# Performance work log

Hardware: AMD Instinct MI355X
Metric: run time of the kernel (lower is better)

Reference implementation:

```python
import jax, jax.numpy as jnp
import numpy as np

EPS = 1e-8
NUM_CELLS = 20
MEM_SIZE = 300
MLP_SIZE = 300
DECAY = 0.98
T, B, H = 512, 128, MEM_SIZE


def setup_inputs() -> dict:
    key = jax.random.key(0)
    ks = jax.random.split(key, 8)
    s = 0.05
    return {
        "hidden_states": jax.random.normal(ks[0], (T, B, H), jnp.float32),
        "input_mask": jnp.ones((T, B), jnp.float32),
        # entity_mlp: H -> MLP_SIZE -> 1
        "We1": jax.random.normal(ks[1], (H, MLP_SIZE), jnp.float32) * s,
        "be1": jnp.zeros((MLP_SIZE,), jnp.float32),
        "We2": jax.random.normal(ks[2], (MLP_SIZE, 1), jnp.float32) * s,
        "be2": jnp.zeros((1,), jnp.float32),
        # sim_mlp: 3H+1 -> MLP_SIZE -> 1
        "Ws1": jax.random.normal(ks[3], (3 * H + 1, MLP_SIZE), jnp.float32) * s,
        "bs1": jnp.zeros((MLP_SIZE,), jnp.float32),
        "Ws2": jax.random.normal(ks[4], (MLP_SIZE, 1), jnp.float32) * s,
        "bs2": jnp.zeros((1,), jnp.float32),
        # U_key: 2H -> H
        "Wu": jax.random.normal(ks[5], (2 * H, H), jnp.float32) * s,
        "bu": jnp.zeros((H,), jnp.float32),
    }


def _forward(hidden_states, input_mask, We1, be1, We2, be2, Ws1, bs1, Ws2, bs2, Wu, bu):
    Tn, Bn, Hn = hidden_states.shape
    M = NUM_CELLS
    # eval-mode random tie-break noise for pick_overwrite_cell (uniform(0.01, 1))
    noise = jax.random.uniform(jax.random.key(42), (Tn, Bn, M), jnp.float32, 0.01, 1.0)

    mem0 = jnp.zeros((Bn, M, Hn), hidden_states.dtype)
    usage0 = jnp.zeros((Bn, M), hidden_states.dtype)

    def step(carry, xs):
        mem, usage = carry
        h, mask, nz = xs  # h: [B,H], mask: [B], nz: [B,M]
        # entity probability: softmax([0, s]) == sigmoid(s)
        ent_score = jnp.maximum(h @ We1 + be1, 0.0) @ We2 + be2  # [B,1]
        ent_prob = jax.nn.sigmoid(ent_score) * mask[:, None]     # [B,1]
        qb = jnp.broadcast_to(h[:, None, :], (Bn, M, Hn))        # [B,M,H]
        pair = jnp.concatenate([mem, qb, qb * mem, usage[..., None]], axis=-1)  # [B,M,3H+1]
        sim = (jnp.maximum(pair @ Ws1 + bs1, 0.0) @ Ws2 + bs2)[..., 0]          # [B,M]
        # coref / overwrite distribution over cells + base slot
        comb = jnp.concatenate([sim, jnp.zeros((Bn, 1), sim.dtype)], axis=1)    # [B,M+1]
        coref_mask = (usage > 0).astype(sim.dtype)
        mult = jnp.concatenate([coref_mask, jnp.ones((Bn, 1), sim.dtype)], axis=1)
        comb = comb * mult + (1.0 - mult) * (-10000.0)
        probs = jax.nn.softmax(comb, axis=1)
        masked = probs * mult
        norm = masked / (jnp.sum(masked, axis=1, keepdims=True) + EPS)
        co = ent_prob * norm
        indv = co[:, :M]                 # [B,M] coref probs
        ow_base = co[:, M:M + 1]         # [B,1] overwrite prob mass
        # pick overwrite cell (eval branch: hard argmax with random tie-break)
        nsim = jax.nn.softmax(sim, axis=-1)
        ow_score = (usage == 0.0).astype(sim.dtype) * nsim * 100000.0 + (1.0 - usage)
        maxv = jnp.max(ow_score, axis=-1, keepdims=True)
        idx = jnp.argmax(nz * (ow_score == maxv).astype(sim.dtype), axis=-1)
        onehot = jax.nn.one_hot(idx, M, dtype=sim.dtype)
        ow = ow_base * onehot            # [B,M]
        # memory candidate + blended update
        cand = jnp.tanh(jnp.concatenate([qb, mem], axis=-1) @ Wu + bu)  # [B,M,H]
        new_mem = (ow[..., None] * qb
                   + (1.0 - ow - indv)[..., None] * mem
                   + indv[..., None] * cand)
        new_usage = jnp.minimum(1.0, ow + indv + DECAY * usage)
        outs = (ent_prob * (1.0 - EPS) + EPS,
                new_usage,
                indv * (1.0 - EPS) + EPS,
                ow * (1.0 - EPS) + EPS)
        return (new_mem, new_usage), outs

    (_, _), (ent, usage_seq, coref, overwrite) = jax.lax.scan(
        step, (mem0, usage0), (hidden_states, input_mask, noise))
    return ent, usage_seq, coref, overwrite


def reference(hidden_states, input_mask, We1, be1, We2, be2, Ws1, bs1, Ws2, bs2, Wu, bu):
    # returns (ent [T,B,1], usage [T,B,M], coref [T,B,M], overwrite [T,B,M])
    return _forward(hidden_states, input_mask, We1, be1, We2, be2,
                    Ws1, bs1, Ws2, bs2, Wu, bu)
```

## Files before the change

kernel.cpp:

```cpp
#include <hip/hip_runtime.h>
#include <math.h>

#define T_STEPS 512
#define BATCH   128
#define HDIM    300
#define M       20
#define M2      10

#define WS_SYNC_FLOATS 16384
#define HB1_OFF  WS_SYNC_FLOATS
#define NTB      (T_STEPS * BATCH)
#define HBUF_FLOATS ((size_t)NTB * HDIM)
#define HWU_OFF  (HB1_OFF + HBUF_FLOATS)
#define ENT_OFF  (HWU_OFF + HBUF_FLOATS)
#define WS_NEED_BYTES ((size_t)(ENT_OFF + NTB) * 4)

__device__ __forceinline__ unsigned rotl32(unsigned v, int r) {
    return (v << r) | (v >> (32 - r));
}

__device__ float jax_noise(unsigned i) {
#pragma clang fp contract(off)
    unsigned x0 = 0u;
    unsigned x1 = i;
    const unsigned ks0 = 0u, ks1 = 42u, ks2 = 0u ^ 42u ^ 0x1BD11BDAu;
    x0 += ks0; x1 += ks1;
    x0 += x1; x1 = rotl32(x1, 13); x1 ^= x0;
    x0 += x1; x1 = rotl32(x1, 15); x1 ^= x0;
    x0 += x1; x1 = rotl32(x1, 26); x1 ^= x0;
    x0 += x1; x1 = rotl32(x1, 6);  x1 ^= x0;
    x0 += ks1; x1 += ks2 + 1u;
    x0 += x1; x1 = rotl32(x1, 17); x1 ^= x0;
    x0 += x1; x1 = rotl32(x1, 29); x1 ^= x0;
    x0 += x1; x1 = rotl32(x1, 16); x1 ^= x0;
    x0 += x1; x1 = rotl32(x1, 24); x1 ^= x0;
    x0 += ks2; x1 += ks0 + 2u;
    x0 += x1; x1 = rotl32(x1, 13); x1 ^= x0;
    x0 += x1; x1 = rotl32(x1, 15); x1 ^= x0;
    x0 += x1; x1 = rotl32(x1, 26); x1 ^= x0;
    x0 += x1; x1 = rotl32(x1, 6);  x1 ^= x0;
    x0 += ks0; x1 += ks1 + 3u;
    x0 += x1; x1 = rotl32(x1, 17); x1 ^= x0;
    x0 += x1; x1 = rotl32(x1, 29); x1 ^= x0;
    x0 += x1; x1 = rotl32(x1, 16); x1 ^= x0;
    x0 += x1; x1 = rotl32(x1, 24); x1 ^= x0;
    x0 += ks1; x1 += ks2 + 4u;
    x0 += x1; x1 = rotl32(x1, 13); x1 ^= x0;
    x0 += x1; x1 = rotl32(x1, 15); x1 ^= x0;
    x0 += x1; x1 = rotl32(x1, 26); x1 ^= x0;
    x0 += x1; x1 = rotl32(x1, 6);  x1 ^= x0;
    x0 += ks2; x1 += ks0 + 5u;

    const unsigned bits = x0 ^ x1;
    const unsigned fb = (bits >> 9) | 0x3f800000u;
    float f = __uint_as_float(fb) - 1.0f;
    const float span = 1.0f - 0.01f;
    float v = f * span;
    v = v + 0.01f;
    return fmaxf(0.01f, v);
}

#define FOR5(X) X(0) X(1) X(2) X(3) X(4)
#define FOR8(X) X(0) X(1) X(2) X(3) X(4) X(5) X(6) X(7)

__global__ void __launch_bounds__(320)
pre_kernel(const float* __restrict__ hs,  const float* __restrict__ msk,
           const float* __restrict__ We1, const float* __restrict__ be1,
           const float* __restrict__ We2, const float* __restrict__ be2,
           const float* __restrict__ Ws1, const float* __restrict__ bs1,
           const float* __restrict__ Wu,  const float* __restrict__ bu,
           float* __restrict__ out, float* __restrict__ ws)
{
    __shared__ __align__(16) float sh_h[8][HDIM];
    __shared__ float sh_ent[5][8];

    float* hb1buf = ws + HB1_OFF;
    float* hwubuf = ws + HWU_OFF;
    float* entbuf = ws + ENT_OFF;

    const int tb0  = blockIdx.x * 8;
    const int tid  = threadIdx.x;
    const int wave = tid >> 6;
    const int lane = tid & 63;
    const int c    = tid;
    const bool act = c < HDIM;

    for (int i = tid; i < 8 * HDIM; i += 320)
        sh_h[i / HDIM][i % HDIM] = hs[(size_t)tb0 * HDIM + i];
    __syncthreads();

    float be1c = 0.f, we2c = 0.f, bs1c = 0.f, buc = 0.f;
    if (act) { be1c = be1[c]; we2c = We2[c]; bs1c = bs1[c]; buc = bu[c]; }

#define DECL(r) float a1_##r = 0.f, ae_##r = 0.f, au_##r = 0.f;
    FOR8(DECL)
#undef DECL
    if (act) {
        const float* q1 = Ws1 + 90000 + c;
        const float* qe = We1 + c;
        const float* qu = Wu + c;
        for (int k = 0; k < HDIM; k += 4) {
            const float* r1 = q1 + k * 300;
            const float* re = qe + k * 300;
            const float* ru = qu + k * 300;
            float w10 = r1[0], w11 = r1[300], w12 = r1[600], w13 = r1[900];
            float e0  = re[0], e1  = re[300], e2  = re[600], e3  = re[900];
            float u0  = ru[0], u1  = ru[300], u2  = ru[600], u3  = ru[900];
#define ACC(r) { float4 h4 = *(const float4*)&sh_h[r][k]; \
            a1_##r += h4.x * w10 + h4.y * w11 + h4.z * w12 + h4.w * w13; \
            ae_##r += h4.x * e0  + h4.y * e1  + h4.z * e2  + h4.w * e3;  \
            au_##r += h4.x * u0  + h4.y * u1  + h4.z * u2  + h4.w * u3; }
            FOR8(ACC)
#undef ACC
        }
#define WR(r) { hb1buf[(size_t)(tb0 + r) * HDIM + c] = a1_##r + bs1c; \
                hwubuf[(size_t)(tb0 + r) * HDIM + c] = au_##r + buc; }
        FOR8(WR)
#undef WR
    }
#define ENT(r) { float er = act ? (fmaxf(ae_##r + be1c, 0.f) * we2c) : 0.f; \
    for (int off = 32; off; off >>= 1) er += __shfl_xor(er, off, 64); \
    if (lane == 0) sh_ent[wave][r] = er; }
    FOR8(ENT)
#undef ENT
    __syncthreads();
    if (tid < 8) {
        float es = sh_ent[0][tid] + sh_ent[1][tid] + sh_ent[2][tid]
                 + sh_ent[3][tid] + sh_ent[4][tid] + be2[0];
        float entp = (1.0f / (1.0f + expf(-es))) * msk[tb0 + tid];
        entbuf[tb0 + tid] = entp;
        out[tb0 + tid] = entp * (1.0f - 1e-8f) + 1e-8f;
    }
}

__global__ void __launch_bounds__(640, 3)
wm_fast(const float* __restrict__ hs,
        const float* __restrict__ We2,
        const float* __restrict__ Ws1,
        const float* __restrict__ Ws2,
        const float* __restrict__ bs2,
        const float* __restrict__ Wu,
        float* __restrict__ out,
        float* __restrict__ ws)
{
    __shared__ __align__(16) float sh_mem[M2][HDIM];
    __shared__ __align__(16) float sh_h[HDIM];
    __shared__ __align__(16) float sh_usage[17408];
    __shared__ float sh_simpart[10][5];
    __shared__ float sh_ow[M];
    __shared__ float sh_indv[M];

    const float* hb1buf = ws + HB1_OFF;
    const float* hwubuf = ws + HWU_OFF;
    const float* entbuf = ws + ENT_OFF;

    const int bid   = blockIdx.x;
    const int b     = bid & 127;
    const int jhalf = bid >> 7;
    const int jb2   = jhalf * 10;
    const int pbase = 10 - jb2;
    const int pbid  = bid ^ 128;

    float*    vals_me = ws + (size_t)bid * 16;
    float*    vals_p  = ws + (size_t)pbid * 16;
    unsigned* flag_me = (unsigned*)(ws + 4096) + (size_t)bid * 16;
    unsigned* flag_p  = (unsigned*)(ws + 4096) + (size_t)pbid * 16;

    const int tid  = threadIdx.x;
    const int wave = tid >> 6;
    const int lane = tid & 63;

    const bool lower   = tid < 320;
    const int  c       = lower ? tid : (tid - 320);
    const bool act     = c < HDIM;
    const int  rowbase = lower ? 0 : 5;

    for (int idx = tid; idx < M2 * HDIM; idx += 640) ((float*)sh_mem)[idx] = 0.0f;
    if (tid < M) sh_usage[tid] = 0.0f;

    const float bs2v = bs2[0];
    float ws2c = 0.f, w900c = 0.f;
    if (act) { ws2c = Ws2[c]; w900c = Ws1[900 * 300 + c]; }
    __syncthreads();

    for (int t = 0; t < T_STEPS; ++t) {
        const int tb = t * BATCH + b;

        if (!lower && act) sh_h[c] = hs[(size_t)tb * HDIM + c];
        __syncthreads();

        const float hb1v = act ? hb1buf[(size_t)tb * HDIM + c] : 0.f;
        const float hwuv = act ? hwubuf[(size_t)tb * HDIM + c] : 0.f;
        const float hreg = act ? sh_h[c] : 0.f;

#define DECL_ACC(jj) float aS_##jj = 0.f, aC_##jj = 0.f;
        FOR5(DECL_ACC)
#undef DECL_ACC
        if (act) {
            const float* qa = Ws1 + c;
            const float* qc = Ws1 + 180000 + c;
            const float* qu = Wu + 90000 + c;
            float A0 = qa[0], A1v = qa[300], A2 = qa[600], A3 = qa[900];
            float C0 = qc[0], C1 = qc[300], C2 = qc[600], C3 = qc[900];
            float U0 = qu[0], U1 = qu[300], U2 = qu[600], U3 = qu[900];
            for (int k = 0; k < HDIM; k += 4) {
                const int kn = (k + 4 < HDIM) ? (k + 4) : 0;
                const float* na = qa + kn * 300;
                const float* nc = qc + kn * 300;
                const float* nu = qu + kn * 300;
                float NA0 = na[0], NA1 = na[300], NA2 = na[600], NA3 = na[900];
                float NC0 = nc[0], NC1 = nc[300], NC2 = nc[600], NC3 = nc[900];
                float NU0 = nu[0], NU1 = nu[300], NU2 = nu[600], NU3 = nu[900];

                float4 h4 = *(const float4*)&sh_h[k];
                float w0 = fmaf(h4.x, C0, A0);
                float w1 = fmaf(h4.y, C1, A1v);
                float w2 = fmaf(h4.z, C2, A2);
                float w3 = fmaf(h4.w, C3, A3);
#define ACC_J(jj) { \
                float4 mv = *(const float4*)&sh_mem[rowbase + jj][k]; \
                aS_##jj += mv.x * w0 + mv.y * w1 + mv.z * w2 + mv.w * w3; \
                aC_##jj += mv.x * U0 + mv.y * U1 + mv.z * U2 + mv.w * U3; }
                FOR5(ACC_J)
#undef ACC_J
                A0 = NA0; A1v = NA1; A2 = NA2; A3 = NA3;
                C0 = NC0; C1 = NC1; C2 = NC2; C3 = NC3;
                U0 = NU0; U1 = NU1; U2 = NU2; U3 = NU3;
            }
        }

        {
            const int gbase = jb2 + rowbase;
#define SIMF(jj) { \
            float v = act ? (fmaxf(aS_##jj + hb1v + sh_usage[gbase + jj] * w900c, 0.0f) * ws2c) : 0.0f; \
            for (int off = 32; off; off >>= 1) v += __shfl_xor(v, off, 64); \
            if (lane == 0) sh_simpart[wave][jj] = v; }
            FOR5(SIMF)
#undef SIMF
        }
        __syncthreads();

        if (wave == 0) {
            float sown = 0.f;
            if (lane < M2) {
                const int wb = (lane < 5) ? 0 : 5;
                const int rr = (lane < 5) ? lane : (lane - 5);
                sown = sh_simpart[wb][rr] + sh_simpart[wb + 1][rr] + sh_simpart[wb + 2][rr]
                     + sh_simpart[wb + 3][rr] + sh_simpart[wb + 4][rr];
                __hip_atomic_store(&vals_me[lane], sown, __ATOMIC_RELAXED,
                                   __HIP_MEMORY_SCOPE_AGENT);
            }
            if (lane == 0) {
                __hip_atomic_store(flag_me, (unsigned)(t + 1), __ATOMIC_RELEASE,
                                   __HIP_MEMORY_SCOPE_AGENT);
                while (__hip_atomic_load(flag_p, __ATOMIC_ACQUIRE,
                                         __HIP_MEMORY_SCOPE_AGENT) < (unsigned)(t + 1))
                    __builtin_amdgcn_s_sleep(1);
            }
            float pvv = 0.f;
            if (lane >= pbase && lane < pbase + M2)
                pvv = __hip_atomic_load(&vals_p[lane - pbase], __ATOMIC_ACQUIRE,
                                        __HIP_MEMORY_SCOPE_AGENT);
            const float myv = __shfl(sown, lane - jb2, 64);

            const bool actc = lane < M;
            const bool own  = actc && (lane >= jb2) && (lane < jb2 + M2);
            float simj = -INFINITY, usg = 0.0f;
            if (actc) {
                simj = (own ? myv : pvv) + bs2v;
                usg  = sh_usage[lane];
            }
            const float entp = entbuf[tb];

            const float coref = (actc && usg > 0.0f) ? 1.0f : 0.0f;
            float comb = actc ? ((usg > 0.0f) ? simj : -10000.0f) : -INFINITY;
            float mx = comb;
            for (int off = 32; off; off >>= 1) mx = fmaxf(mx, __shfl_xor(mx, off, 64));
            mx = fmaxf(mx, 0.0f);
            float e = actc ? expf(comb - mx) : 0.0f;
            const float eM = expf(0.0f - mx);
            float den = e;
            for (int off = 32; off; off >>= 1) den += __shfl_xor(den, off, 64);
            den += eM;
            const float prob  = e / den;
            const float probM = eM / den;
            float masked = prob * coref;
            float msum = masked;
            for (int off = 32; off; off >>= 1) msum += __shfl_xor(msum, off, 64);
            msum += probM;
            const float dn = msum + 1e-8f;
            const float normj = masked / dn;
            const float normM = probM / dn;
            const float indv = actc ? (entp * normj) : 0.0f;
            const float ow_base = entp * normM;

            float nmx = simj;
            for (int off = 32; off; off >>= 1) nmx = fmaxf(nmx, __shfl_xor(nmx, off, 64));
            float ne = actc ? expf(simj - nmx) : 0.0f;
            float ns = ne;
            for (int off = 32; off; off >>= 1) ns += __shfl_xor(ns, off, 64);
            const float nsim = ne / ns;

            float ows = actc ? (((usg == 0.0f) ? nsim * 100000.0f : 0.0f) + (1.0f - usg))
                             : -INFINITY;
            float mv = ows;
            for (int off = 32; off; off >>= 1) mv = fmaxf(mv, __shfl_xor(mv, off, 64));

            float key = 0.0f;
            if (actc && ows == mv) key = jax_noise((unsigned)(tb * M + lane));
            float bv = actc ? key : -1.0f;
            int bi = actc ? lane : 1023;
            for (int off = 32; off; off >>= 1) {
                float ov = __shfl_xor(bv, off, 64);
                int oi = __shfl_xor(bi, off, 64);
                if (ov > bv || (ov == bv && oi < bi)) { bv = ov; bi = oi; }
            }
            const float ow = (actc && lane == bi) ? ow_base : 0.0f;
            const float nu = fminf(1.0f, (ow + indv) + 0.98f * usg);

            if (actc) {
                sh_ow[lane] = ow;
                sh_indv[lane] = indv;
                sh_usage[lane] = nu;
            }
            if (own) {
                const int base = tb * M + lane;
                out[65536 + base]   = nu;
                out[1376256 + base] = indv * (1.0f - 1e-8f) + 1e-8f;
                out[2686976 + base] = ow * (1.0f - 1e-8f) + 1e-8f;
            }
        }
        __syncthreads();

        if (act) {
            const int gbase = jb2 + rowbase;
#define DUPD(jj) { \
            const float owj = sh_ow[gbase + jj]; \
            const float inj = sh_indv[gbase + jj]; \
            const float cd  = tanhf(aC_##jj + hwuv); \
            const float mo  = sh_mem[rowbase + jj][c]; \
            sh_mem[rowbase + jj][c] = owj * hreg + (1.0f - owj - inj) * mo + inj * cd; }
            FOR5(DUPD)
#undef DUPD
        }
    }
}

__global__ void __launch_bounds__(640, 3)
wm_kernel(const float* __restrict__ hs, const float* __restrict__ msk,
          const float* __restrict__ We1, const float* __restrict__ be1,
          const float* __restrict__ We2, const float* __restrict__ be2,
          const float* __restrict__ Ws1, const float* __restrict__ bs1,
          const float* __restrict__ Ws2, const float* __restrict__ bs2,
          const float* __restrict__ Wu,  const float* __restrict__ bu,
          float* __restrict__ out, float* __restrict__ ws)
{
    __shared__ __align__(16) float sh_mem[M2][HDIM];
    __shared__ __align__(16) float sh_h[HDIM];
    __shared__ __align__(16) float sh_hb1[HDIM];
    __shared__ __align__(16) float sh_hwu[HDIM];
    __shared__ __align__(16) float sh_usage[16384];
    __shared__ float sh_simpart[10][5];
    __shared__ float sh_entpart[5];
    __shared__ float sh_ow[M];
    __shared__ float sh_indv[M];

    const int bid   = blockIdx.x;
    const int b     = bid & 127;
    const int jhalf = bid >> 7;
    const int jb2   = jhalf * 10;
    const int pbase = 10 - jb2;
    const int pbid  = bid ^ 128;

    float*    vals_me = ws + (size_t)bid * 16;
    float*    vals_p  = ws + (size_t)pbid * 16;
    unsigned* flag_me = (unsigned*)(ws + 4096) + (size_t)bid * 16;
    unsigned* flag_p  = (unsigned*)(ws + 4096) + (size_t)pbid * 16;

    const int tid  = threadIdx.x;
    const int wave = tid >> 6;
    const int lane = tid & 63;

    const bool lower   = tid < 320;
    const int  c       = lower ? tid : (tid - 320);
    const bool act     = c < HDIM;
    const int  rowbase = lower ? 0 : 5;

    for (int idx = tid; idx < M2 * HDIM; idx += 640) ((float*)sh_mem)[idx] = 0.0f;
    if (tid < M) sh_usage[tid] = 0.0f;

    const float be2v = be2[0];
    const float bs2v = bs2[0];
    float bs1c = 0.f, be1c = 0.f, we2c = 0.f, ws2c = 0.f, w900c = 0.f, buc = 0.f;
    if (act) {
        ws2c  = Ws2[c];
        w900c = Ws1[900 * 300 + c];
        if (lower) { bs1c = bs1[c]; be1c = be1[c]; we2c = We2[c]; }
        else       { buc = bu[c]; }
    }
    __syncthreads();

    for (int t = 0; t < T_STEPS; ++t) {
        const int tb = t * BATCH + b;

        if (!lower && act) sh_h[c] = hs[(size_t)tb * HDIM + c];
        __syncthreads();

        float hb1reg = 0.f, hwureg = 0.f;
        if (lower) {
            float a1 = 0.f, ae = 0.f;
            if (act) {
                const float* q  = Ws1 + 90000 + c;
                const float* qe = We1 + c;
                float Q0 = q[0], Q1 = q[300], Q2 = q[600], Q3 = q[900];
                float E0 = qe[0], E1 = qe[300], E2 = qe[600], E3 = qe[900];
                for (int k = 0; k < HDIM; k += 4) {
                    const int kn = (k + 4 < HDIM) ? (k + 4) : 0;
                    const float* nq = q + kn * 300;
                    const float* nE = qe + kn * 300;
                    float NQ0 = nq[0], NQ1 = nq[300], NQ2 = nq[600], NQ3 = nq[900];
                    float NE0 = nE[0], NE1 = nE[300], NE2 = nE[600], NE3 = nE[900];
                    float4 h4 = *(const float4*)&sh_h[k];
                    a1 += h4.x * Q0 + h4.y * Q1 + h4.z * Q2 + h4.w * Q3;
                    ae += h4.x * E0 + h4.y * E1 + h4.z * E2 + h4.w * E3;
                    Q0 = NQ0; Q1 = NQ1; Q2 = NQ2; Q3 = NQ3;
                    E0 = NE0; E1 = NE1; E2 = NE2; E3 = NE3;
                }
            }
            float er = act ? (fmaxf(ae + be1c, 0.0f) * we2c) : 0.0f;
            for (int off = 32; off; off >>= 1) er += __shfl_xor(er, off, 64);
            if (lane == 0) sh_entpart[wave] = er;
            hb1reg = a1 + bs1c;
            if (act) sh_hb1[c] = hb1reg;
        } else {
            float au = 0.f;
            if (act) {
                const float* qu = Wu + c;
                float U0 = qu[0], U1 = qu[300], U2 = qu[600], U3 = qu[900];
                for (int k = 0; k < HDIM; k += 4) {
                    const int kn = (k + 4 < HDIM) ? (k + 4) : 0;
                    const float* nu = qu + kn * 300;
                    float NU0 = nu[0], NU1 = nu[300], NU2 = nu[600], NU3 = nu[900];
                    float4 h4 = *(const float4*)&sh_h[k];
                    au += h4.x * U0 + h4.y * U1 + h4.z * U2 + h4.w * U3;
                    U0 = NU0; U1 = NU1; U2 = NU2; U3 = NU3;
                }
            }
            hwureg = au + buc;
            if (act) sh_hwu[c] = hwureg;
        }

#define DECL_ACC(jj) float aS_##jj = 0.f, aC_##jj = 0.f;
        FOR5(DECL_ACC)
#undef DECL_ACC
        if (act) {
            const float* qa = Ws1 + c;
            const float* qc = Ws1 + 180000 + c;
            const float* qu = Wu + 90000 + c;
            float A0 = qa[0], A1v = qa[300], A2 = qa[600], A3 = qa[900];
            float C0 = qc[0], C1 = qc[300], C2 = qc[600], C3 = qc[900];
            float U0 = qu[0], U1 = qu[300], U2 = qu[600], U3 = qu[900];
            for (int k = 0; k < HDIM; k += 4) {
                const int kn = (k + 4 < HDIM) ? (k + 4) : 0;
                const float* na = qa + kn * 300;
                const float* nc = qc + kn * 300;
                const float* nu = qu + kn * 300;
                float NA0 = na[0], NA1 = na[300], NA2 = na[600], NA3 = na[900];
                float NC0 = nc[0], NC1 = nc[300], NC2 = nc[600], NC3 = nc[900];
                float NU0 = nu[0], NU1 = nu[300], NU2 = nu[600], NU3 = nu[900];
                float4 h4 = *(const float4*)&sh_h[k];
                float w0 = fmaf(h4.x, C0, A0);
                float w1 = fmaf(h4.y, C1, A1v);
                float w2 = fmaf(h4.z, C2, A2);
                float w3 = fmaf(h4.w, C3, A3);
#define ACC_J(jj) { \
                float4 mv = *(const float4*)&sh_mem[rowbase + jj][k]; \
                aS_##jj += mv.x * w0 + mv.y * w1 + mv.z * w2 + mv.w * w3; \
                aC_##jj += mv.x * U0 + mv.y * U1 + mv.z * U2 + mv.w * U3; }
                FOR5(ACC_J)
#undef ACC_J
                A0 = NA0; A1v = NA1; A2 = NA2; A3 = NA3;
                C0 = NC0; C1 = NC1; C2 = NC2; C3 = NC3;
                U0 = NU0; U1 = NU1; U2 = NU2; U3 = NU3;
            }
        }
        __syncthreads();

        const float hreg  = act ? sh_h[c] : 0.f;
        const float myhb1 = lower ? hb1reg : (act ? sh_hb1[c] : 0.f);
        const float myhwu = lower ? (act ? sh_hwu[c] : 0.f) : hwureg;

        {
            const int gbase = jb2 + rowbase;
#define SIMF(jj) { \
            float v = act ? (fmaxf(aS_##jj + myhb1 + sh_usage[gbase + jj] * w900c, 0.0f) * ws2c) : 0.0f; \
            for (int off = 32; off; off >>= 1) v += __shfl_xor(v, off, 64); \
            if (lane == 0) sh_simpart[wave][jj] = v; }
            FOR5(SIMF)
#undef SIMF
        }
        __syncthreads();

        if (wave == 0) {
            float sown = 0.f;
            if (lane < M2) {
                const int wb = (lane < 5) ? 0 : 5;
                const int rr = (lane < 5) ? lane : (lane - 5);
                sown = sh_simpart[wb][rr] + sh_simpart[wb + 1][rr] + sh_simpart[wb + 2][rr]
                     + sh_simpart[wb + 3][rr] + sh_simpart[wb + 4][rr];
                __hip_atomic_store(&vals_me[lane], sown, __ATOMIC_RELAXED,
                                   __HIP_MEMORY_SCOPE_AGENT);
            }
            if (lane == 0) {
                __hip_atomic_store(flag_me, (unsigned)(t + 1), __ATOMIC_RELEASE,
                                   __HIP_MEMORY_SCOPE_AGENT);
                while (__hip_atomic_load(flag_p, __ATOMIC_ACQUIRE,
                                         __HIP_MEMORY_SCOPE_AGENT) < (unsigned)(t + 1))
                    __builtin_amdgcn_s_sleep(1);
            }
            float pvv = 0.f;
            if (lane >= pbase && lane < pbase + M2)
                pvv = __hip_atomic_load(&vals_p[lane - pbase], __ATOMIC_ACQUIRE,
                                        __HIP_MEMORY_SCOPE_AGENT);
            const float myv = __shfl(sown, lane - jb2, 64);

            const bool actc = lane < M;
            const bool own  = actc && (lane >= jb2) && (lane < jb2 + M2);
            float simj = -INFINITY, usg = 0.0f;
            if (actc) {
                simj = (own ? myv : pvv) + bs2v;
                usg  = sh_usage[lane];
            }
            float es = sh_entpart[0] + sh_entpart[1] + sh_entpart[2]
                     + sh_entpart[3] + sh_entpart[4] + be2v;
            const float entp = (1.0f / (1.0f + expf(-es))) * msk[tb];

            const float coref = (actc && usg > 0.0f) ? 1.0f : 0.0f;
            float comb = actc ? ((usg > 0.0f) ? simj : -10000.0f) : -INFINITY;
            float mx = comb;
            for (int off = 32; off; off >>= 1) mx = fmaxf(mx, __shfl_xor(mx, off, 64));
            mx = fmaxf(mx, 0.0f);
            float e = actc ? expf(comb - mx) : 0.0f;
            const float eM = expf(0.0f - mx);
            float den = e;
            for (int off = 32; off; off >>= 1) den += __shfl_xor(den, off, 64);
            den += eM;
            const float prob  = e / den;
            const float probM = eM / den;
            float masked = prob * coref;
            float msum = masked;
            for (int off = 32; off; off >>= 1) msum += __shfl_xor(msum, off, 64);
            msum += probM;
            const float dn = msum + 1e-8f;
            const float normj = masked / dn;
            const float normM = probM / dn;
            const float indv = actc ? (entp * normj) : 0.0f;
            const float ow_base = entp * normM;

            float nmx = simj;
            for (int off = 32; off; off >>= 1) nmx = fmaxf(nmx, __shfl_xor(nmx, off, 64));
            float ne = actc ? expf(simj - nmx) : 0.0f;
            float ns = ne;
            for (int off = 32; off; off >>= 1) ns += __shfl_xor(ns, off, 64);
            const float nsim = ne / ns;

            float ows = actc ? (((usg == 0.0f) ? nsim * 100000.0f : 0.0f) + (1.0f - usg))
                             : -INFINITY;
            float mv = ows;
            for (int off = 32; off; off >>= 1) mv = fmaxf(mv, __shfl_xor(mv, off, 64));

            float key = 0.0f;
            if (actc && ows == mv) key = jax_noise((unsigned)(tb * M + lane));
            float bv = actc ? key : -1.0f;
            int bi = actc ? lane : 1023;
            for (int off = 32; off; off >>= 1) {
                float ov = __shfl_xor(bv, off, 64);
                int oi = __shfl_xor(bi, off, 64);
                if (ov > bv || (ov == bv && oi < bi)) { bv = ov; bi = oi; }
            }
            const float ow = (actc && lane == bi) ? ow_base : 0.0f;
            const float nu = fminf(1.0f, (ow + indv) + 0.98f * usg);

            if (actc) {
                sh_ow[lane] = ow;
                sh_indv[lane] = indv;
                sh_usage[lane] = nu;
            }
            if (own) {
                const int base = tb * M + lane;
                out[65536 + base]   = nu;
                out[1376256 + base] = indv * (1.0f - 1e-8f) + 1e-8f;
                out[2686976 + base] = ow * (1.0f - 1e-8f) + 1e-8f;
            }
            if (jhalf == 0 && lane == 0) out[tb] = entp * (1.0f - 1e-8f) + 1e-8f;
        }
        __syncthreads();

        if (act) {
            const int gbase = jb2 + rowbase;
#define DUPD(jj) { \
            const float owj = sh_ow[gbase + jj]; \
            const float inj = sh_indv[gbase + jj]; \
            const float cd  = tanhf(aC_##jj + myhwu); \
            const float mo  = sh_mem[rowbase + jj][c]; \
            sh_mem[rowbase + jj][c] = owj * hreg + (1.0f - owj - inj) * mo + inj * cd; }
            FOR5(DUPD)
#undef DUPD
        }
    }
}

extern "C" void kernel_launch(void* const* d_in, const int* in_sizes, int n_in,
                              void* d_out, int out_size, void* d_ws, size_t ws_size,
                              hipStream_t stream) {
    (void)in_sizes; (void)n_in; (void)out_size;
    const float* hs  = (const float*)d_in[0];
    const float* msk = (const float*)d_in[1];
    const float* We1 = (const float*)d_in[2];
    const float* be1 = (const float*)d_in[3];
    const float* We2 = (const float*)d_in[4];
    const float* be2 = (const float*)d_in[5];
    const float* Ws1 = (const float*)d_in[6];
    const float* bs1 = (const float*)d_in[7];
    const float* Ws2 = (const float*)d_in[8];
    const float* bs2 = (const float*)d_in[9];
    const float* Wu  = (const float*)d_in[10];
    const float* bu  = (const float*)d_in[11];
    float* out = (float*)d_out;

    hipMemsetAsync(d_ws, 0, 64 * 1024, stream);
    if (ws_size >= WS_NEED_BYTES) {
        hipLaunchKernelGGL(pre_kernel, dim3(NTB / 8), dim3(320), 0, stream,
                           hs, msk, We1, be1, We2, be2, Ws1, bs1, Wu, bu,
                           out, (float*)d_ws);
        hipLaunchKernelGGL(wm_fast, dim3(256), dim3(640), 0, stream,
                           hs, We2, Ws1, Ws2, bs2, Wu, out, (float*)d_ws);
    } else {
        hipLaunchKernelGGL(wm_kernel, dim3(256), dim3(640), 0, stream,
                           hs, msk, We1, be1, We2, be2, Ws1, bs1, Ws2, bs2, Wu, bu,
                           out, (float*)d_ws);
    }
}
```

Baseline: 17.82 ms.

## Split K across wave pairs and compute two columns per thread in sim/cand matvec

The per-step sim and candidate matvec is reorganised. Each thread now computes two adjacent output columns using float2 weight loads. Even and odd waves each handle one half of the K range, and the partial sums go to new shared-memory buffers. The sim and tanh epilogues then add the two halves, which costs an extra __syncthreads and a larger shared-memory footprint. The sh_usage buffer was shrunk to make room. The intent is to reuse each mem/h LDS read across two columns and to balance work better across all 640 threads.

```diff
diff --git a/kernel.cpp b/kernel.cpp
--- a/kernel.cpp
+++ b/kernel.cpp
@@ -145,7 +145,9 @@
 {
     __shared__ __align__(16) float sh_mem[M2][HDIM];
     __shared__ __align__(16) float sh_h[HDIM];
-    __shared__ __align__(16) float sh_usage[17408];
+    __shared__ __align__(16) float sh_simS[2][M2][HDIM];
+    __shared__ __align__(16) float sh_candS[2][M2][HDIM];
+    __shared__ __align__(16) float sh_usage[5632];
     __shared__ float sh_simpart[10][5];
     __shared__ float sh_ow[M];
     __shared__ float sh_indv[M];
@@ -175,6 +177,16 @@
     const bool act     = c < HDIM;
     const int  rowbase = lower ? 0 : 5;
 
+    const int  sB   = wave & 1;
+    const int  idxB = (wave >> 1) * 64 + lane;
+    const bool actB = idxB < 300;
+    const int  g2   = idxB / 150;
+    const int  pB   = idxB % 150;
+    const int  c0   = 2 * pB;
+    const int  jl   = g2 * 5;
+    const int  kbeg = sB ? 152 : 0;
+    const int  kend = sB ? 300 : 152;
+
     for (int idx = tid; idx < M2 * HDIM; idx += 640) ((float*)sh_mem)[idx] = 0.0f;
     if (tid < M) sh_usage[tid] = 0.0f;
 
@@ -193,46 +205,84 @@
         const float hwuv = act ? hwubuf[(size_t)tb * HDIM + c] : 0.f;
         const float hreg = act ? sh_h[c] : 0.f;
 
-#define DECL_ACC(jj) float aS_##jj = 0.f, aC_##jj = 0.f;
+#define DECL_ACC(jj) float aS0_##jj = 0.f, aS1_##jj = 0.f, aC0_##jj = 0.f, aC1_##jj = 0.f;
         FOR5(DECL_ACC)
 #undef DECL_ACC
-        if (act) {
-            const float* qa = Ws1 + c;
-            const float* qc = Ws1 + 180000 + c;
-            const float* qu = Wu + 90000 + c;
-            float A0 = qa[0], A1v = qa[300], A2 = qa[600], A3 = qa[900];
-            float C0 = qc[0], C1 = qc[300], C2 = qc[600], C3 = qc[900];
-            float U0 = qu[0], U1 = qu[300], U2 = qu[600], U3 = qu[900];
-            for (int k = 0; k < HDIM; k += 4) {
-                const int kn = (k + 4 < HDIM) ? (k + 4) : 0;
+        if (actB) {
+            const float* qa = Ws1 + c0;
+            const float* qc = Ws1 + 180000 + c0;
+            const float* qu = Wu + 90000 + c0;
+            const float* ia = qa + kbeg * 300;
+            const float* ic = qc + kbeg * 300;
+            const float* iu = qu + kbeg * 300;
+            float2 A0 = *(const float2*)(ia);
+            float2 A1 = *(const float2*)(ia + 300);
+            float2 A2 = *(const float2*)(ia + 600);
+            float2 A3 = *(const float2*)(ia + 900);
+            float2 C0 = *(const float2*)(ic);
+            float2 C1 = *(const float2*)(ic + 300);
+            float2 C2 = *(const float2*)(ic + 600);
+            float2 C3 = *(const float2*)(ic + 900);
+            float2 U0 = *(const float2*)(iu);
+            float2 U1 = *(const float2*)(iu + 300);
+            float2 U2 = *(const float2*)(iu + 600);
+            float2 U3 = *(const float2*)(iu + 900);
+            for (int k = kbeg; k < kend; k += 4) {
+                const int kn = (k + 4 < kend) ? (k + 4) : kbeg;
                 const float* na = qa + kn * 300;
                 const float* nc = qc + kn * 300;
                 const float* nu = qu + kn * 300;
-                float NA0 = na[0], NA1 = na[300], NA2 = na[600], NA3 = na[900];
-                float NC0 = nc[0], NC1 = nc[300], NC2 = nc[600], NC3 = nc[900];
-                float NU0 = nu[0], NU1 = nu[300], NU2 = nu[600], NU3 = nu[900];
+                float2 NA0 = *(const float2*)(na);
+                float2 NA1 = *(const float2*)(na + 300);
+                float2 NA2 = *(const float2*)(na + 600);
+                float2 NA3 = *(const float2*)(na + 900);
+                float2 NC0 = *(const float2*)(nc);
+                float2 NC1 = *(const float2*)(nc + 300);
+                float2 NC2 = *(const float2*)(nc + 600);
+                float2 NC3 = *(const float2*)(nc + 900);
+                float2 NU0 = *(const float2*)(nu);
+                float2 NU1 = *(const float2*)(nu + 300);
+                float2 NU2 = *(const float2*)(nu + 600);
+                float2 NU3 = *(const float2*)(nu + 900);
 
                 float4 h4 = *(const float4*)&sh_h[k];
-                float w0 = fmaf(h4.x, C0, A0);
-                float w1 = fmaf(h4.y, C1, A1v);
-                float w2 = fmaf(h4.z, C2, A2);
-                float w3 = fmaf(h4.w, C3, A3);
+                float w00 = fmaf(h4.x, C0.x, A0.x);
+                float w01 = fmaf(h4.y, C1.x, A1.x);
+                float w02 = fmaf(h4.z, C2.x, A2.x);
+                float w03 = fmaf(h4.w, C3.x, A3.x);
+                float w10 = fmaf(h4.x, C0.y, A0.y);
+                float w11 = fmaf(h4.y, C1.y, A1.y);
+                float w12 = fmaf(h4.z, C2.y, A2.y);
+                float w13 = fmaf(h4.w, C3.y, A3.y);
 #define ACC_J(jj) { \
-                float4 mv = *(const float4*)&sh_mem[rowbase + jj][k]; \
-                aS_##jj += mv.x * w0 + mv.y * w1 + mv.z * w2 + mv.w * w3; \
-                aC_##jj += mv.x * U0 + mv.y * U1 + mv.z * U2 + mv.w * U3; }
+                float4 mv = *(const float4*)&sh_mem[jl + jj][k]; \
+                aS0_##jj += mv.x * w00 + mv.y * w01 + mv.z * w02 + mv.w * w03; \
+                aS1_##jj += mv.x * w10 + mv.y * w11 + mv.z * w12 + mv.w * w13; \
+                aC0_##jj += mv.x * U0.x + mv.y * U1.x + mv.z * U2.x + mv.w * U3.x; \
+                aC1_##jj += mv.x * U0.y + mv.y * U1.y + mv.z * U2.y + mv.w * U3.y; }
                 FOR5(ACC_J)
 #undef ACC_J
-                A0 = NA0; A1v = NA1; A2 = NA2; A3 = NA3;
+                A0 = NA0; A1 = NA1; A2 = NA2; A3 = NA3;
                 C0 = NC0; C1 = NC1; C2 = NC2; C3 = NC3;
                 U0 = NU0; U1 = NU1; U2 = NU2; U3 = NU3;
             }
-        }
+#define WB(jj) { \
+            *(float2*)&sh_simS[sB][jl + jj][c0]  = make_float2(aS0_##jj, aS1_##jj); \
+            *(float2*)&sh_candS[sB][jl + jj][c0] = make_float2(aC0_##jj, aC1_##jj); }
+            FOR5(WB)
+#undef WB
+        }
+        __syncthreads();
 
         {
             const int gbase = jb2 + rowbase;
 #define SIMF(jj) { \
-            float v = act ? (fmaxf(aS_##jj + hb1v + sh_usage[gbase + jj] * w900c, 0.0f) * ws2c) : 0.0f; \
+            float v = 0.f; \
+            if (act) { \
+                float pre = sh_simS[0][rowbase + jj][c] + sh_simS[1][rowbase + jj][c] \
+                          + hb1v + sh_usage[gbase + jj] * w900c; \
+                v = fmaxf(pre, 0.0f) * ws2c; \
+            } \
             for (int off = 32; off; off >>= 1) v += __shfl_xor(v, off, 64); \
             if (lane == 0) sh_simpart[wave][jj] = v; }
             FOR5(SIMF)
@@ -337,7 +387,8 @@
 #define DUPD(jj) { \
             const float owj = sh_ow[gbase + jj]; \
             const float inj = sh_indv[gbase + jj]; \
-            const float cd  = tanhf(aC_##jj + hwuv); \
+            const float cd  = tanhf(sh_candS[0][rowbase + jj][c] \
+                                  + sh_candS[1][rowbase + jj][c] + hwuv); \
             const float mo  = sh_mem[rowbase + jj][c]; \
             sh_mem[rowbase + jj][c] = owj * hreg + (1.0f - owj - inj) * mo + inj * cd; }
             FOR5(DUPD)
```

Result: slower. 21.64 ms (+21.4%).
